# Kernel optimization log

Hardware: AMD Instinct MI355X
Metric: run time of the kernel (lower is better)

Reference implementation:

```python
import jax, jax.numpy as jnp
import numpy as np

B, T, S, H, V = 2, 512, 400, 1024, 50257


def setup_inputs() -> dict:
    key = jax.random.key(0)
    ks = jax.random.split(key, 5)
    x = jax.random.normal(ks[0], (B, T, H), dtype=jnp.float32)
    attn_dist = jax.random.normal(ks[1], (B, T, S), dtype=jnp.float32)
    enc_batch_extend_vocab = jax.random.randint(ks[2], (B, S), 0, V)
    # learned params of nn.Linear(H, V) and nn.Linear(H, 1)
    proj_w = jax.random.normal(ks[3], (V, H), dtype=jnp.float32) * 0.02
    proj_b = jnp.zeros((V,), dtype=jnp.float32)
    pgen_w = jax.random.normal(ks[4], (1, H), dtype=jnp.float32) * 0.02
    pgen_b = jnp.zeros((1,), dtype=jnp.float32)
    return {
        "x": x,
        "attn_dist": attn_dist,
        "enc_batch_extend_vocab": enc_batch_extend_vocab,
        "temp": 1,
        "proj_w": proj_w,
        "proj_b": proj_b,
        "pgen_w": pgen_w,
        "pgen_b": pgen_b,
    }


def reference(x, attn_dist, enc_batch_extend_vocab, temp, proj_w, proj_b, pgen_w, pgen_b):
    # p_gen gate: sigmoid(Linear(H -> 1))  -> [B, T, 1]
    p_gen = jax.nn.sigmoid(jnp.einsum("bth,oh->bto", x, pgen_w) + pgen_b)
    # vocab projection: [B, T, V]
    logit = jnp.einsum("bth,vh->btv", x, proj_w) + proj_b
    vocab_dist = jax.nn.softmax(logit / temp, axis=2)
    vocab_dist_ = p_gen * vocab_dist  # [B, T, V]
    # copy distribution over source tokens: [B, T, S]
    attn = jax.nn.softmax(attn_dist / temp, axis=-1)
    attn_ = (1.0 - p_gen) * attn
    # scatter_add along vocab dim; source ids broadcast over decode steps
    idx = jnp.broadcast_to(enc_batch_extend_vocab[:, None, :], attn_.shape)  # [B, T, S]
    scat = jax.vmap(jax.vmap(lambda vd, ix, a: vd.at[ix].add(a)))
    out = scat(vocab_dist_, idx, attn_)
    return jnp.log(out + 1e-40)
```

## Files before the change

kernel.cpp:

```cpp
#include <hip/hip_runtime.h>
#include <hip/hip_bf16.h>

#define BB 2
#define TT 512
#define SS 400
#define HH 1024
#define VV 50257
#define MM (BB*TT)

#define NTILE 393
#define NT_PAD 400
#define VPAD 50304

typedef __attribute__((ext_vector_type(8))) short short8;
typedef __attribute__((ext_vector_type(4))) float f32x4;

#define AS1 __attribute__((address_space(1)))
#define AS3 __attribute__((address_space(3)))

static __device__ __forceinline__ void gl_lds16(const unsigned short* g, unsigned short* l) {
    __builtin_amdgcn_global_load_lds((const AS1 unsigned int*)(g), (AS3 unsigned int*)(l), 16, 0, 0);
}

static __device__ __forceinline__ unsigned short f2bf(float f) {
    union { float f; unsigned u; } x;
    x.f = f;
    unsigned r = x.u + 0x7FFFu + ((x.u >> 16) & 1u);
    return (unsigned short)(r >> 16);
}

static __device__ __forceinline__ float bf2f(unsigned short u) {
    union { unsigned u; float f; } x;
    x.u = ((unsigned)u) << 16;
    return x.f;
}

static __device__ __forceinline__ float get_invtemp(const int* tp) {
    int iv = *tp;
    float f;
    if (iv > 0 && iv < 100000) f = (float)iv;
    else                       f = __int_as_float(iv);
    return 1.0f / f;
}

__global__ void zero1_k(int* a, int na) {
    int i = blockIdx.x * blockDim.x + threadIdx.x;
    int st = gridDim.x * blockDim.x;
    for (int t = i; t < na; t += st) a[t] = 0;
}

__global__ void cvtx_pgen_k(const float* __restrict__ x, const float* __restrict__ pw,
                            const float* __restrict__ pb, unsigned short* __restrict__ xb,
                            float* __restrict__ pgen) {
    int m = blockIdx.x, tid = threadIdx.x;
    float4 v = ((const float4*)(x + (size_t)m * HH))[tid];
    ushort4 o;
    o.x = f2bf(v.x); o.y = f2bf(v.y); o.z = f2bf(v.z); o.w = f2bf(v.w);
    ((ushort4*)(xb + (size_t)m * HH))[tid] = o;
    float4 w4 = ((const float4*)pw)[tid];
    float s = v.x * w4.x + v.y * w4.y + v.z * w4.z + v.w * w4.w;
    for (int off = 32; off; off >>= 1) s += __shfl_down(s, off);
    __shared__ float red[4];
    if ((tid & 63) == 0) red[tid >> 6] = s;
    __syncthreads();
    if (tid == 0) {
        float t = red[0] + red[1] + red[2] + red[3] + pb[0];
        pgen[m] = 1.0f / (1.0f + __expf(-t));
    }
}

__global__ void cvt_w_k(const float* __restrict__ W, unsigned short* __restrict__ Wb) {
    size_t g = (size_t)blockIdx.x * 256 + threadIdx.x;
    size_t e0 = g * 8;
    int v = (int)(e0 >> 10);
    short8 o;
    if (v < VV) {
        float4 a = *(const float4*)(W + e0);
        float4 b = *(const float4*)(W + e0 + 4);
        o[0] = f2bf(a.x); o[1] = f2bf(a.y); o[2] = f2bf(a.z); o[3] = f2bf(a.w);
        o[4] = f2bf(b.x); o[5] = f2bf(b.y); o[6] = f2bf(b.z); o[7] = f2bf(b.w);
    } else {
        o = (short8){0,0,0,0,0,0,0,0};
    }
    *(short8*)(Wb + e0) = o;
}

__global__ void map_build_k(const int* __restrict__ enc, int* __restrict__ mapv) {
    int t = blockIdx.x * blockDim.x + threadIdx.x;
    if (t >= BB * SS) return;
    int b = t / SS, s = t % SS;
    int id = enc[b * SS + s];
    atomicCAS(&mapv[(size_t)b * VV + id], 0, s + 1);
}

__global__ void attn_k(const float* __restrict__ attn, const int* __restrict__ enc,
                       const int* __restrict__ mapv, const float* __restrict__ pgen,
                       float* __restrict__ Aacc, const int* __restrict__ tempp) {
    int m = blockIdx.x, tid = threadIdx.x;
    int b = m >> 9;
    float invt = get_invtemp(tempp);
    __shared__ float sv[SS];
    __shared__ float ev[SS];
    __shared__ int   slt[SS];
    __shared__ float red[256];
    float loc = -1e30f;
    for (int s = tid; s < SS; s += 256) {
        float v = attn[(size_t)m * SS + s] * invt;
        sv[s] = v;
        loc = fmaxf(loc, v);
    }
    red[tid] = loc; __syncthreads();
    for (int h = 128; h; h >>= 1) { if (tid < h) red[tid] = fmaxf(red[tid], red[tid + h]); __syncthreads(); }
    float mx = red[0]; __syncthreads();
    float ls = 0.f;
    for (int s = tid; s < SS; s += 256) {
        float e = __expf(sv[s] - mx);
        ev[s] = e;
        ls += e;
        slt[s] = mapv[(size_t)b * VV + enc[b * SS + s]] - 1;
    }
    red[tid] = ls; __syncthreads();
    for (int h = 128; h; h >>= 1) { if (tid < h) red[tid] += red[tid + h]; __syncthreads(); }
    float scale = (1.0f - pgen[m]) / red[0];
    for (int s0 = tid; s0 < SS; s0 += 256) {
        float a = 0.f;
        for (int s = 0; s < SS; ++s)
            a += (slt[s] == s0) ? ev[s] : 0.f;
        Aacc[(size_t)m * SS + s0] = a * scale;
    }
}

template<int LOGBF>
__global__ __launch_bounds__(256) void gemm9_k(
    const unsigned short* __restrict__ xb, const unsigned short* __restrict__ Wb,
    const float* __restrict__ bias, float* __restrict__ outf,
    unsigned short* __restrict__ outb,
    float* __restrict__ pmax, float* __restrict__ psum,
    const int* __restrict__ tempp) {
    __shared__ unsigned short As0[128 * 32];
    __shared__ unsigned short Bs0[128 * 32];
    __shared__ unsigned short As1[128 * 32];
    __shared__ unsigned short Bs1[128 * 32];
    __shared__ float red_mx[2][2][64];
    __shared__ float red_sm[2][2][64];

    int wgid = blockIdx.x;
    int xcd = wgid & 7;
    int l = wgid >> 3;
    int nt = xcd * 50 + (l >> 3);
    int mt = l & 7;
    if (nt >= NTILE) return;
    int m0 = mt * 128, n0 = nt * 128;

    int tid = threadIdx.x;
    int lane = tid & 63, w = tid >> 6;
    int wr = w >> 1, wc = w & 1;
    int r15 = lane & 15, kg = lane >> 4;

    size_t aoff[2], boff[2];
    int ldst[2];
#pragma unroll
    for (int i = 0; i < 2; i++) {
        int q = i * 256 + tid;
        int row = q >> 2, jc = q & 3;
        aoff[i] = (size_t)(m0 + row) * HH + jc * 8;
        boff[i] = (size_t)(n0 + row) * HH + jc * 8;
        ldst[i] = q * 8;
    }

    f32x4 acc[4][4];
#pragma unroll
    for (int i = 0; i < 4; i++)
#pragma unroll
        for (int j = 0; j < 4; j++) acc[i][j] = (f32x4){0.f, 0.f, 0.f, 0.f};

#define STAGE(A_, B_, k0_) do { \
    _Pragma("unroll") for (int i_ = 0; i_ < 2; i_++) { \
        gl_lds16(xb + aoff[i_] + (k0_), (A_) + ldst[i_]); \
        gl_lds16(Wb + boff[i_] + (k0_), (B_) + ldst[i_]); \
    } } while (0)
#define COMPUTE(A_, B_) do { \
    short8 af_[4], bf_[4]; \
    _Pragma("unroll") for (int mi_ = 0; mi_ < 4; mi_++) \
        af_[mi_] = *(const short8*)&(A_)[(wr * 64 + mi_ * 16 + r15) * 32 + kg * 8]; \
    _Pragma("unroll") for (int ni_ = 0; ni_ < 4; ni_++) \
        bf_[ni_] = *(const short8*)&(B_)[(wc * 64 + ni_ * 16 + r15) * 32 + kg * 8]; \
    _Pragma("unroll") for (int mi_ = 0; mi_ < 4; mi_++) \
    _Pragma("unroll") for (int ni_ = 0; ni_ < 4; ni_++) \
        acc[mi_][ni_] = __builtin_amdgcn_mfma_f32_16x16x32_bf16(af_[mi_], bf_[ni_], acc[mi_][ni_], 0, 0, 0); \
    } while (0)

    STAGE(As0, Bs0, 0);
    __syncthreads();

    for (int p = 0; p < 16; ++p) {
        int k2 = p * 64;
        STAGE(As1, Bs1, k2 + 32);
        COMPUTE(As0, Bs0);
        __syncthreads();
        if (p < 15) STAGE(As0, Bs0, k2 + 64);
        COMPUTE(As1, Bs1);
        __syncthreads();
    }
#undef STAGE
#undef COMPUTE

    float invt = get_invtemp(tempp);
    float bv[4]; bool vld[4]; int gn[4];
#pragma unroll
    for (int ni = 0; ni < 4; ni++) {
        gn[ni] = n0 + wc * 64 + ni * 16 + r15;
        vld[ni] = gn[ni] < VV;
        bv[ni] = vld[ni] ? bias[gn[ni]] : 0.f;
    }
#pragma unroll
    for (int mi = 0; mi < 4; mi++) {
#pragma unroll
        for (int j = 0; j < 4; j++) {
            float mx = -1e30f;
#pragma unroll
            for (int ni = 0; ni < 4; ni++)
                if (vld[ni]) mx = fmaxf(mx, (acc[mi][ni][j] + bv[ni]) * invt);
            float sm = 0.f;
#pragma unroll
            for (int ni = 0; ni < 4; ni++)
                if (vld[ni]) sm += __expf((acc[mi][ni][j] + bv[ni]) * invt - mx);
#pragma unroll
            for (int o = 1; o < 16; o <<= 1) {
                float m2 = __shfl_xor(mx, o);
                float s2 = __shfl_xor(sm, o);
                float nm = fmaxf(mx, m2);
                sm = sm * __expf(mx - nm) + s2 * __expf(m2 - nm);
                mx = nm;
            }
            if (r15 == 0) {
                red_mx[wr][wc][mi * 16 + kg * 4 + j] = mx;
                red_sm[wr][wc][mi * 16 + kg * 4 + j] = sm;
            }
        }
    }
#pragma unroll
    for (int ni = 0; ni < 4; ni++) {
        if (vld[ni]) {
#pragma unroll
            for (int mi = 0; mi < 4; mi++) {
                int gmb = m0 + wr * 64 + mi * 16 + (kg << 2);
#pragma unroll
                for (int j = 0; j < 4; j++) {
                    if (LOGBF)
                        outb[(size_t)(gmb + j) * VPAD + gn[ni]] = f2bf(acc[mi][ni][j] + bv[ni]);
                    else
                        outf[(size_t)(gmb + j) * VV + gn[ni]] = acc[mi][ni][j] + bv[ni];
                }
            }
        }
    }
    __syncthreads();
    if (tid < 128) {
        int r = tid & 63, wr2 = tid >> 6;
        float m1 = red_mx[wr2][0][r], s1 = red_sm[wr2][0][r];
        float m2 = red_mx[wr2][1][r], s2 = red_sm[wr2][1][r];
        float nm = fmaxf(m1, m2);
        float s = s1 * __expf(m1 - nm) + s2 * __expf(m2 - nm);
        int gm = m0 + wr2 * 64 + r;
        pmax[(size_t)gm * NT_PAD + nt] = nm;
        psum[(size_t)gm * NT_PAD + nt] = s;
    }
}

__global__ void lse_wave_k(const float* __restrict__ pmax, const float* __restrict__ psum,
                           float* __restrict__ lse) {
    int gw = (blockIdx.x * blockDim.x + threadIdx.x) >> 6;
    int ln = threadIdx.x & 63;
    if (gw >= MM) return;
    const float* pm = pmax + (size_t)gw * NT_PAD;
    const float* ps = psum + (size_t)gw * NT_PAD;
    float M = -1e30f, S = 0.f;
    for (int t = ln; t < NTILE; t += 64) {
        float m2 = pm[t], s2 = ps[t];
        float nm = fmaxf(M, m2);
        S = S * __expf(M - nm) + s2 * __expf(m2 - nm);
        M = nm;
    }
#pragma unroll
    for (int o = 1; o < 64; o <<= 1) {
        float m2 = __shfl_xor(M, o);
        float s2 = __shfl_xor(S, o);
        float nm = fmaxf(M, m2);
        S = S * __expf(M - nm) + s2 * __expf(m2 - nm);
        M = nm;
    }
    if (ln == 0) lse[gw] = M + __logf(S);
}

__global__ void finalize_bf_k(const unsigned short* __restrict__ logb,
                              float* __restrict__ out, const float* __restrict__ pgen,
                              const float* __restrict__ lse, const int* __restrict__ mapv,
                              const float* __restrict__ Aacc, const int* __restrict__ tempp) {
    int m = blockIdx.y;
    int c = blockIdx.x * 256 + threadIdx.x;
    int v0 = c * 4;
    if (v0 >= VV) return;
    int b = m >> 9;
    float invt = get_invtemp(tempp);
    float pg = pgen[m], L = lse[m];
    ushort4 lb = *(const ushort4*)(logb + (size_t)m * VPAD + v0);
    const int* mrow = mapv + (size_t)b * VV;
    const float* arow = Aacc + (size_t)m * SS;
    size_t base = (size_t)m * VV;
    unsigned short ls[4] = {lb.x, lb.y, lb.z, lb.w};
#pragma unroll
    for (int j = 0; j < 4; j++) {
        int v = v0 + j;
        if (v < VV) {
            float p = pg * __expf(bf2f(ls[j]) * invt - L);
            int jm = mrow[v];
            if (jm) p += arow[jm - 1];
            out[base + v] = __logf(p + 1e-40f);
        }
    }
}

__global__ void finalize_k(float* __restrict__ out, const float* __restrict__ pgen,
                           const float* __restrict__ lse, const int* __restrict__ mapv,
                           const float* __restrict__ Aacc, const int* __restrict__ tempp) {
    int m = blockIdx.y;
    int b = m >> 9;
    float invt = get_invtemp(tempp);
    float pg = pgen[m], L = lse[m];
    size_t base = (size_t)m * VV;
    const int* mrow = mapv + (size_t)b * VV;
    const float* arow = Aacc + (size_t)m * SS;
    int sk = (-m) & 3;
    int nchunk = (VV - sk) >> 2;
    int c = blockIdx.x * 256 + threadIdx.x;
    if (c < nchunk) {
        int v0 = sk + 4 * c;
        float4 l4 = *(const float4*)(out + base + v0);
        float xs[4] = {l4.x, l4.y, l4.z, l4.w};
        float rs[4];
#pragma unroll
        for (int j = 0; j < 4; j++) {
            float p = pg * __expf(xs[j] * invt - L);
            int jm = mrow[v0 + j];
            if (jm) p += arow[jm - 1];
            rs[j] = __logf(p + 1e-40f);
        }
        float4 o4 = {rs[0], rs[1], rs[2], rs[3]};
        *(float4*)(out + base + v0) = o4;
    }
    if (blockIdx.x == 0 && threadIdx.x == 0) {
        for (int v = 0; v < sk; v++) {
            float p = pg * __expf(out[base + v] * invt - L);
            int jm = mrow[v];
            if (jm) p += arow[jm - 1];
            out[base + v] = __logf(p + 1e-40f);
        }
        for (int v = sk + 4 * nchunk; v < VV; v++) {
            float p = pg * __expf(out[base + v] * invt - L);
            int jm = mrow[v];
            if (jm) p += arow[jm - 1];
            out[base + v] = __logf(p + 1e-40f);
        }
    }
}

__global__ __launch_bounds__(256) void gemm_old_k(
    const unsigned short* __restrict__ xb, const float* __restrict__ W,
    const float* __restrict__ bias, float* __restrict__ out) {
    __shared__ unsigned short As[128][40];
    __shared__ unsigned short Bs[128][40];
    int bid = blockIdx.x;
    int mt = bid & 7;
    int nt = bid >> 3;
    int m0 = mt * 128, n0 = nt * 128;
    int tid = threadIdx.x;
    int lid = tid & 63, w = tid >> 6;
    int wr = w >> 1, wc = w & 1;
    int row16 = lid & 15, kg = lid >> 4;

    f32x4 acc[4][4];
#pragma unroll
    for (int i = 0; i < 4; i++)
#pragma unroll
        for (int j = 0; j < 4; j++) acc[i][j] = (f32x4){0.f, 0.f, 0.f, 0.f};

    int tr = tid >> 3;
    int tc = (tid & 7) << 2;

    for (int kt = 0; kt < HH / 32; ++kt) {
        int k0 = kt * 32;
        __syncthreads();
#pragma unroll
        for (int i = 0; i < 4; i++) {
            int r = tr + 32 * i;
            ushort4 a4 = *(const ushort4*)&xb[(size_t)(m0 + r) * HH + k0 + tc];
            *(ushort4*)&As[r][tc] = a4;
            int v = n0 + r; v = (v < VV) ? v : (VV - 1);
            float4 w4 = *(const float4*)&W[(size_t)v * HH + k0 + tc];
            ushort4 b4;
            b4.x = f2bf(w4.x); b4.y = f2bf(w4.y); b4.z = f2bf(w4.z); b4.w = f2bf(w4.w);
            *(ushort4*)&Bs[r][tc] = b4;
        }
        __syncthreads();
        short8 af[4], bf[4];
#pragma unroll
        for (int i = 0; i < 4; i++) {
            af[i] = *(const short8*)&As[wr * 64 + i * 16 + row16][kg * 8];
            bf[i] = *(const short8*)&Bs[wc * 64 + i * 16 + row16][kg * 8];
        }
#pragma unroll
        for (int mi = 0; mi < 4; mi++)
#pragma unroll
            for (int ni = 0; ni < 4; ni++)
                acc[mi][ni] = __builtin_amdgcn_mfma_f32_16x16x32_bf16(af[mi], bf[ni], acc[mi][ni], 0, 0, 0);
    }
#pragma unroll
    for (int ni = 0; ni < 4; ni++) {
        int gnv = n0 + wc * 64 + ni * 16 + row16;
        if (gnv < VV) {
            float bvv = bias[gnv];
#pragma unroll
            for (int mi = 0; mi < 4; mi++) {
                int gmb = m0 + wr * 64 + mi * 16 + (kg << 2);
#pragma unroll
                for (int j = 0; j < 4; j++)
                    out[(size_t)(gmb + j) * VV + gnv] = acc[mi][ni][j] + bvv;
            }
        }
    }
}

__global__ void rowreduce_k(const float* __restrict__ out, float* __restrict__ lse,
                            const int* __restrict__ tempp) {
    int m = blockIdx.x, tid = threadIdx.x;
    float invt = get_invtemp(tempp);
    const float* row = out + (size_t)m * VV;
    int sk = (-m) & 3;
    int nchunk = (VV - sk) >> 2;
    float mi = -1e30f, si = 0.f;
    for (int c = tid; c < nchunk; c += 256) {
        float4 x4 = *(const float4*)(row + sk + 4 * c);
        float xs[4] = {x4.x, x4.y, x4.z, x4.w};
#pragma unroll
        for (int j = 0; j < 4; j++) {
            float x = xs[j] * invt;
            float nm = fmaxf(mi, x);
            si = si * __expf(mi - nm) + __expf(x - nm);
            mi = nm;
        }
    }
    if (tid == 0) {
        for (int v = 0; v < sk; v++) {
            float x = row[v] * invt;
            float nm = fmaxf(mi, x);
            si = si * __expf(mi - nm) + __expf(x - nm);
            mi = nm;
        }
        for (int v = sk + 4 * nchunk; v < VV; v++) {
            float x = row[v] * invt;
            float nm = fmaxf(mi, x);
            si = si * __expf(mi - nm) + __expf(x - nm);
            mi = nm;
        }
    }
    __shared__ float sm[256], ss[256];
    sm[tid] = mi; ss[tid] = si; __syncthreads();
    for (int h = 128; h; h >>= 1) {
        if (tid < h) {
            float m2 = sm[tid + h], s2 = ss[tid + h];
            float nm = fmaxf(sm[tid], m2);
            ss[tid] = ss[tid] * __expf(sm[tid] - nm) + s2 * __expf(m2 - nm);
            sm[tid] = nm;
        }
        __syncthreads();
    }
    if (tid == 0) lse[m] = sm[0] + __logf(ss[0]);
}

extern "C" void kernel_launch(void* const* d_in, const int* in_sizes, int n_in,
                              void* d_out, int out_size, void* d_ws, size_t ws_size,
                              hipStream_t stream) {
    const float* x      = (const float*)d_in[0];
    const float* attn   = (const float*)d_in[1];
    const int*   enc    = (const int*)d_in[2];
    const int*   temp   = (const int*)d_in[3];
    const float* proj_w = (const float*)d_in[4];
    const float* proj_b = (const float*)d_in[5];
    const float* pgen_w = (const float*)d_in[6];
    const float* pgen_b = (const float*)d_in[7];
    float* out = (float*)d_out;

    char* ws = (char*)d_ws;
    const size_t WB_BYTES = (size_t)VPAD * HH * 2;

    size_t o_wb   = 0;
    size_t o_xb   = o_wb + WB_BYTES;
    size_t o_pgen = o_xb + 2097152;
    size_t o_lse  = o_pgen + 4096;
    size_t o_map  = o_lse + 4096;
    size_t o_aacc = o_map + 402432;
    size_t o_pmax = o_aacc + (size_t)MM * SS * 4;
    size_t o_psum = o_pmax + (size_t)MM * NT_PAD * 4;
    size_t o_logb = o_psum + (size_t)MM * NT_PAD * 4;
    size_t need_mid = o_logb;
    size_t need_big = o_logb + (size_t)MM * VPAD * 2;

    if (ws_size >= need_mid) {
        unsigned short* wb   = (unsigned short*)(ws + o_wb);
        unsigned short* xb   = (unsigned short*)(ws + o_xb);
        float*          pgen = (float*)(ws + o_pgen);
        float*          lse  = (float*)(ws + o_lse);
        int*            mapv = (int*)(ws + o_map);
        float*          Aacc = (float*)(ws + o_aacc);
        float*          pmax = (float*)(ws + o_pmax);
        float*          psum = (float*)(ws + o_psum);
        unsigned short* logb = (unsigned short*)(ws + o_logb);

        zero1_k<<<256, 256, 0, stream>>>(mapv, BB * VV);
        cvtx_pgen_k<<<MM, 256, 0, stream>>>(x, pgen_w, pgen_b, xb, pgen);
        cvt_w_k<<<(VPAD * HH / 8 + 255) / 256, 256, 0, stream>>>(proj_w, wb);
        map_build_k<<<4, 256, 0, stream>>>(enc, mapv);
        attn_k<<<MM, 256, 0, stream>>>(attn, enc, mapv, pgen, Aacc, temp);
        if (ws_size >= need_big) {
            gemm9_k<1><<<8 * NT_PAD, 256, 0, stream>>>(xb, wb, proj_b, out, logb, pmax, psum, temp);
            lse_wave_k<<<256, 256, 0, stream>>>(pmax, psum, lse);
            finalize_bf_k<<<dim3((VV + 1023) / 1024, MM), 256, 0, stream>>>(logb, out, pgen, lse, mapv, Aacc, temp);
        } else {
            gemm9_k<0><<<8 * NT_PAD, 256, 0, stream>>>(xb, wb, proj_b, out, logb, pmax, psum, temp);
            lse_wave_k<<<256, 256, 0, stream>>>(pmax, psum, lse);
            finalize_k<<<dim3(50, MM), 256, 0, stream>>>(out, pgen, lse, mapv, Aacc, temp);
        }
    } else {
        unsigned short* xb   = (unsigned short*)(ws + 0);
        float*          pgen = (float*)(ws + 2097152);
        float*          lse  = (float*)(ws + 2101248);
        int*            mapv = (int*)(ws + 2105344);
        float*          Aacc = (float*)(ws + 2507776);

        zero1_k<<<256, 256, 0, stream>>>(mapv, BB * VV);
        cvtx_pgen_k<<<MM, 256, 0, stream>>>(x, pgen_w, pgen_b, xb, pgen);
        map_build_k<<<4, 256, 0, stream>>>(enc, mapv);
        attn_k<<<MM, 256, 0, stream>>>(attn, enc, mapv, pgen, Aacc, temp);
        gemm_old_k<<<8 * NTILE, 256, 0, stream>>>(xb, proj_w, proj_b, out);
        rowreduce_k<<<MM, 256, 0, stream>>>(out, lse, temp);
        finalize_k<<<dim3(50, MM), 256, 0, stream>>>(out, pgen, lse, mapv, Aacc, temp);
    }
}
```

Baseline: 473.6 us.

## Deepen GEMM K-tile to 64 with XOR-swizzled LDS and manual waitcnt pipelining

The bf16 MFMA GEMM now stages 64-wide K tiles instead of 32 and XOR-swizzles the LDS layout to avoid bank conflicts on fragment reads. Fragments are loaded into registers before the next global-to-LDS stage is issued. Synchronisation uses explicit vmcnt/lgkmcnt waits and raw s_barrier with sched barriers, replacing __syncthreads. This halves the number of barriers per K step and overlaps loads with MFMA work, at the cost of doubled LDS use (about 64KB), which may reduce occupancy, and more fragment registers.

```diff
diff --git a/kernel.cpp b/kernel.cpp
--- a/kernel.cpp
+++ b/kernel.cpp
@@ -17,6 +17,13 @@
 
 #define AS1 __attribute__((address_space(1)))
 #define AS3 __attribute__((address_space(3)))
+
+#define SBAR()  do { asm volatile("s_barrier" ::: "memory"); \
+                     __builtin_amdgcn_sched_barrier(0); } while (0)
+#define WAITV(n) do { asm volatile("s_waitcnt vmcnt(" #n ")" ::: "memory"); \
+                      __builtin_amdgcn_sched_barrier(0); } while (0)
+#define WAITL0() do { asm volatile("s_waitcnt lgkmcnt(0)" ::: "memory"); \
+                      __builtin_amdgcn_sched_barrier(0); } while (0)
 
 static __device__ __forceinline__ void gl_lds16(const unsigned short* g, unsigned short* l) {
     __builtin_amdgcn_global_load_lds((const AS1 unsigned int*)(g), (AS3 unsigned int*)(l), 16, 0, 0);
@@ -131,16 +138,16 @@
 }
 
 template<int LOGBF>
-__global__ __launch_bounds__(256) void gemm9_k(
+__global__ __launch_bounds__(256) void gemm10_k(
     const unsigned short* __restrict__ xb, const unsigned short* __restrict__ Wb,
     const float* __restrict__ bias, float* __restrict__ outf,
     unsigned short* __restrict__ outb,
     float* __restrict__ pmax, float* __restrict__ psum,
     const int* __restrict__ tempp) {
-    __shared__ unsigned short As0[128 * 32];
-    __shared__ unsigned short Bs0[128 * 32];
-    __shared__ unsigned short As1[128 * 32];
-    __shared__ unsigned short Bs1[128 * 32];
+    __shared__ unsigned short As0[128 * 64];
+    __shared__ unsigned short Bs0[128 * 64];
+    __shared__ unsigned short As1[128 * 64];
+    __shared__ unsigned short Bs1[128 * 64];
     __shared__ float red_mx[2][2][64];
     __shared__ float red_sm[2][2][64];
 
@@ -157,15 +164,16 @@
     int wr = w >> 1, wc = w & 1;
     int r15 = lane & 15, kg = lane >> 4;
 
-    size_t aoff[2], boff[2];
-    int ldst[2];
-#pragma unroll
-    for (int i = 0; i < 2; i++) {
+    size_t aoff[4], boff[4];
+    int ldst[4];
+#pragma unroll
+    for (int i = 0; i < 4; i++) {
         int q = i * 256 + tid;
-        int row = q >> 2, jc = q & 3;
+        int row = q >> 3;
+        int jc = (q & 7) ^ (row & 7);
         aoff[i] = (size_t)(m0 + row) * HH + jc * 8;
         boff[i] = (size_t)(n0 + row) * HH + jc * 8;
-        ldst[i] = q * 8;
+        ldst[i] = (i * 256 + w * 64) * 8;
     }
 
     f32x4 acc[4][4];
@@ -175,35 +183,63 @@
         for (int j = 0; j < 4; j++) acc[i][j] = (f32x4){0.f, 0.f, 0.f, 0.f};
 
 #define STAGE(A_, B_, k0_) do { \
-    _Pragma("unroll") for (int i_ = 0; i_ < 2; i_++) { \
+    _Pragma("unroll") for (int i_ = 0; i_ < 4; i_++) { \
         gl_lds16(xb + aoff[i_] + (k0_), (A_) + ldst[i_]); \
         gl_lds16(Wb + boff[i_] + (k0_), (B_) + ldst[i_]); \
     } } while (0)
-#define COMPUTE(A_, B_) do { \
-    short8 af_[4], bf_[4]; \
-    _Pragma("unroll") for (int mi_ = 0; mi_ < 4; mi_++) \
-        af_[mi_] = *(const short8*)&(A_)[(wr * 64 + mi_ * 16 + r15) * 32 + kg * 8]; \
-    _Pragma("unroll") for (int ni_ = 0; ni_ < 4; ni_++) \
-        bf_[ni_] = *(const short8*)&(B_)[(wc * 64 + ni_ * 16 + r15) * 32 + kg * 8]; \
+#define LOADFRAG(AF_, BF_, A_, B_) do { \
+    _Pragma("unroll") for (int h_ = 0; h_ < 2; h_++) { \
+        _Pragma("unroll") for (int mi_ = 0; mi_ < 4; mi_++) { \
+            int row_ = wr * 64 + mi_ * 16 + r15; \
+            int jc_ = ((h_ << 2) | kg) ^ (row_ & 7); \
+            AF_[h_ * 4 + mi_] = *(const short8*)&(A_)[row_ * 64 + jc_ * 8]; \
+        } \
+        _Pragma("unroll") for (int ni_ = 0; ni_ < 4; ni_++) { \
+            int row_ = wc * 64 + ni_ * 16 + r15; \
+            int jc_ = ((h_ << 2) | kg) ^ (row_ & 7); \
+            BF_[h_ * 4 + ni_] = *(const short8*)&(B_)[row_ * 64 + jc_ * 8]; \
+        } \
+    } } while (0)
+#define MFMA32(AF_, BF_) do { \
+    _Pragma("unroll") for (int h_ = 0; h_ < 2; h_++) \
     _Pragma("unroll") for (int mi_ = 0; mi_ < 4; mi_++) \
     _Pragma("unroll") for (int ni_ = 0; ni_ < 4; ni_++) \
-        acc[mi_][ni_] = __builtin_amdgcn_mfma_f32_16x16x32_bf16(af_[mi_], bf_[ni_], acc[mi_][ni_], 0, 0, 0); \
+        acc[mi_][ni_] = __builtin_amdgcn_mfma_f32_16x16x32_bf16( \
+            AF_[h_ * 4 + mi_], BF_[h_ * 4 + ni_], acc[mi_][ni_], 0, 0, 0); \
     } while (0)
 
     STAGE(As0, Bs0, 0);
-    __syncthreads();
-
-    for (int p = 0; p < 16; ++p) {
-        int k2 = p * 64;
-        STAGE(As1, Bs1, k2 + 32);
-        COMPUTE(As0, Bs0);
-        __syncthreads();
-        if (p < 15) STAGE(As0, Bs0, k2 + 64);
-        COMPUTE(As1, Bs1);
-        __syncthreads();
-    }
+    STAGE(As1, Bs1, 64);
+
+    short8 af[8], bf[8];
+    for (int p = 0; p < 7; ++p) {
+        int k4 = p * 128;
+        WAITV(8);
+        SBAR();
+        LOADFRAG(af, bf, As0, Bs0);
+        WAITL0();
+        SBAR();
+        STAGE(As0, Bs0, k4 + 128);
+        MFMA32(af, bf);
+        WAITV(8);
+        SBAR();
+        LOADFRAG(af, bf, As1, Bs1);
+        WAITL0();
+        SBAR();
+        STAGE(As1, Bs1, k4 + 192);
+        MFMA32(af, bf);
+    }
+    WAITV(8);
+    SBAR();
+    LOADFRAG(af, bf, As0, Bs0);
+    MFMA32(af, bf);
+    WAITV(0);
+    SBAR();
+    LOADFRAG(af, bf, As1, Bs1);
+    MFMA32(af, bf);
 #undef STAGE
-#undef COMPUTE
+#undef LOADFRAG
+#undef MFMA32
 
     float invt = get_invtemp(tempp);
     float bv[4]; bool vld[4]; int gn[4];
@@ -523,11 +559,11 @@
         map_build_k<<<4, 256, 0, stream>>>(enc, mapv);
         attn_k<<<MM, 256, 0, stream>>>(attn, enc, mapv, pgen, Aacc, temp);
         if (ws_size >= need_big) {
-            gemm9_k<1><<<8 * NT_PAD, 256, 0, stream>>>(xb, wb, proj_b, out, logb, pmax, psum, temp);
+            gemm10_k<1><<<8 * NT_PAD, 256, 0, stream>>>(xb, wb, proj_b, out, logb, pmax, psum, temp);
             lse_wave_k<<<256, 256, 0, stream>>>(pmax, psum, lse);
             finalize_bf_k<<<dim3((VV + 1023) / 1024, MM), 256, 0, stream>>>(logb, out, pgen, lse, mapv, Aacc, temp);
         } else {
-            gemm9_k<0><<<8 * NT_PAD, 256, 0, stream>>>(xb, wb, proj_b, out, logb, pmax, psum, temp);
+            gemm10_k<0><<<8 * NT_PAD, 256, 0, stream>>>(xb, wb, proj_b, out, logb, pmax, psum, temp);
             lse_wave_k<<<256, 256, 0, stream>>>(pmax, psum, lse);
             finalize_k<<<dim3(50, MM), 256, 0, stream>>>(out, pgen, lse, mapv, Aacc, temp);
         }
```

Result: faster. 431.0 us (-9.0%).
